# Optimization experiments

Hardware: AMD Instinct MI355X
Metric: run time of the kernel (lower is better)

## Reference

```python
import jax, jax.numpy as jnp
import numpy as np

VOCAB, EMB, HID = 50000, 128, 256
B, T = 64, 512


def setup_inputs() -> dict:
    key = jax.random.key(0)
    ks = jax.random.split(key, 10)
    node = jax.random.randint(ks[0], (B, T, 2), 0, VOCAB, dtype=jnp.int32)
    rel = jax.random.randint(ks[1], (B, T, 3), 0, VOCAB, dtype=jnp.int32)
    father = jax.random.randint(ks[2], (B, T), 0, T, dtype=jnp.int32)
    mask = jnp.ones((B, T), jnp.float32)
    # parameters (PyTorch LSTM layout: gates ordered i,f,g,o)
    embedding = jax.random.normal(ks[3], (VOCAB, EMB), jnp.float32) * 1e-4
    W_ih = jax.random.uniform(ks[4], (4 * HID, 2 * EMB), jnp.float32, -0.02, 0.02)
    W_hh = jax.random.uniform(ks[5], (4 * HID, HID), jnp.float32, -0.02, 0.02)
    b_ih = jnp.zeros((4 * HID,), jnp.float32).at[HID:2 * HID].set(1.0)  # forget bias = 1
    b_hh = jnp.zeros((4 * HID,), jnp.float32)
    W_h = jax.random.normal(ks[6], (HID, HID), jnp.float32) * 0.02
    return {"src_gtr_seq_node": node, "src_gtr_seq_rel": rel,
            "src_gtr_seq_father": father, "src_gtr_seq_node_mask": mask,
            "embedding": embedding, "W_ih": W_ih, "W_hh": W_hh,
            "b_ih": b_ih, "b_hh": b_hh, "W_h": W_h}


def reference(src_gtr_seq_node, src_gtr_seq_rel, src_gtr_seq_father,
              src_gtr_seq_node_mask, embedding, W_ih, W_hh, b_ih, b_hh, W_h):
    node, rel, father, mask = (src_gtr_seq_node, src_gtr_seq_rel,
                               src_gtr_seq_father, src_gtr_seq_node_mask)
    Bn, Tn = node.shape[:2]
    H = W_hh.shape[1]
    t_idx = jnp.arange(Tn, dtype=jnp.int32)
    # valid parent at step t must point into memory slots [0..t]; -1 -> zero root slot
    father = jnp.minimum(father, (t_idx - 1)[None, :])
    # 'avg' mode: mean of first-2 node token embeddings, mean of rel token embeddings
    node_e = embedding[node].mean(axis=2)            # [B,T,E]
    rel_e = embedding[rel].mean(axis=2)              # [B,T,E]
    x = jnp.concatenate([node_e, rel_e], axis=-1)    # [B,T,2E]
    gx = jnp.einsum('bte,ge->btg', x, W_ih) + b_ih   # [B,T,4H] input-side gates
    barange = jnp.arange(Bn)
    h_mem0 = jnp.zeros((Tn + 1, Bn, H), x.dtype)     # slot 0 = zero state (root)
    c_mem0 = jnp.zeros((Tn + 1, Bn, H), x.dtype)

    def step(carry, inp):
        h_mem, c_mem = carry
        t, gx_t, f_t = inp
        h_prev = h_mem[f_t + 1, barange]             # parent gather [B,H]
        c_prev = c_mem[f_t + 1, barange]
        gates = gx_t + h_prev @ W_hh.T + b_hh        # [B,4H]
        i, f, g, o = jnp.split(gates, 4, axis=-1)
        c = jax.nn.sigmoid(f) * c_prev + jax.nn.sigmoid(i) * jnp.tanh(g)
        h = jax.nn.sigmoid(o) * jnp.tanh(c)
        return (h_mem.at[t + 1].set(h), c_mem.at[t + 1].set(c)), h

    (h_mem, c_mem), outs = jax.lax.scan(
        step, (h_mem0, c_mem0),
        (t_idx, gx.transpose(1, 0, 2), father.T))
    m = mask[:, :, None]
    encoder_outputs = outs.transpose(1, 0, 2) * m    # [B,T,H]
    encoder_feature = encoder_outputs.reshape(-1, H) @ W_h.T  # [B*T,H]
    h_max = (h_mem[1:].transpose(1, 0, 2) * m).max(axis=1)[None]  # [1,B,H]
    c_max = (c_mem[1:].transpose(1, 0, 2) * m).max(axis=1)[None]
    return encoder_outputs, encoder_feature, h_max, c_max
```

## Files before the change

kernel.cpp:

```cpp
#include <hip/hip_runtime.h>
#include <hip/hip_bf16.h>
#include <math.h>

#define NB 64
#define NT 512
#define NH 256
#define NG 1024

typedef __bf16 bf16x8 __attribute__((ext_vector_type(8)));
typedef float  f32x4  __attribute__((ext_vector_type(4)));
typedef unsigned int u32x2 __attribute__((ext_vector_type(2)));

static __device__ __forceinline__ unsigned short f2bf(float x){
  __hip_bfloat16 h = __float2bfloat16(x);
  return __builtin_bit_cast(unsigned short, h);
}
static __device__ __forceinline__ float bf2f(unsigned short u){
  return __bfloat162float(__builtin_bit_cast(__hip_bfloat16, u));
}

#if __has_builtin(__builtin_amdgcn_sdot4)
#define SDOT4(a,b,c) __builtin_amdgcn_sdot4((a),(b),(c),false)
#else
static __device__ __forceinline__ int SDOT4(int a, int b, int c){
  c += ((a<<24)>>24)*((b<<24)>>24);
  c += ((a<<16)>>24)*((b<<16)>>24);
  c += ((a<< 8)>>24)*((b<< 8)>>24);
  c += ( a     >>24)*( b     >>24);
  return c;
}
#endif

#define QRED(x) do {                                                      \
    x += __builtin_amdgcn_update_dpp(0, x, 0xB1, 0xF, 0xF, true);         \
    x += __builtin_amdgcn_update_dpp(0, x, 0x4E, 0xF, 0xF, true);         \
  } while(0)

#define BAR_LGKM() asm volatile("s_waitcnt lgkmcnt(0)\n\ts_barrier" ::: "memory")
#define BAR_ALL()  asm volatile("s_waitcnt vmcnt(0) lgkmcnt(0)\n\ts_barrier" ::: "memory")

#define PIN(x) asm volatile("" : "+v"(x))

static __device__ __forceinline__ float tanh_acc(float x){
  float ax = fabsf(x);
  if (ax < 0.04f){
    float x2 = x*x;
    return x * (1.0f + x2*(-(1.0f/3.0f) + x2*(2.0f/15.0f)));
  }
  float e = __expf(-2.0f*ax);
  float r = (1.0f - e) / (1.0f + e);
  return copysignf(r, x);
}
static __device__ __forceinline__ float sigm(float x){
  return 1.0f / (1.0f + __expf(-x));
}

#define HSCALE 1270000.0f
#define WSCALE 6350.0f
#define DQ_CONST (1.0f/(HSCALE*WSCALE))

__global__ __launch_bounds__(256) void k_prep(
    const float* __restrict__ Wih, const float* __restrict__ Whh,
    const float* __restrict__ Wh,  const float* __restrict__ bih,
    const float* __restrict__ bhh,
    unsigned short* __restrict__ wih_bf, unsigned short* __restrict__ wh_bf,
    int* __restrict__ wq, float* __restrict__ bias)
{
  int i = blockIdx.x*256 + threadIdx.x;
  wih_bf[i] = f2bf(Wih[i]);
  if (i < 65536){
    wh_bf[i] = f2bf(Wh[i]);
    float4 wv = *(const float4*)(Whh + (long)i*4);
    int q0 = (int)rintf(wv.x * WSCALE); q0 = max(-127, min(127, q0));
    int q1 = (int)rintf(wv.y * WSCALE); q1 = max(-127, min(127, q1));
    int q2 = (int)rintf(wv.z * WSCALE); q2 = max(-127, min(127, q2));
    int q3 = (int)rintf(wv.w * WSCALE); q3 = max(-127, min(127, q3));
    int packed = (q0&255) | ((q1&255)<<8) | ((q2&255)<<16) | ((q3&255)<<24);
    int R = i >> 6, j = i & 63;
    int gate = R >> 8, ug = R & 255;
    int wv_ = ug >> 5, ul = ug & 31;
    int grp = ul >> 1, s = ul & 1;
    int ck = j >> 4, k = j & 15;
    int lane2 = grp*4 + ck;
    int r = gate*2 + s;
    wq[(((long)wv_*64 + lane2)*8 + r)*16 + k] = packed;
  }
  if (i < 1024) bias[i] = bih[i] + bhh[i];
}

__global__ __launch_bounds__(128) void k_x(
    const int* __restrict__ node, const int* __restrict__ rel,
    const float* __restrict__ emb, unsigned short* __restrict__ x)
{
  int bt = blockIdx.x; int e = threadIdx.x;
  int n0 = node[bt*2+0], n1 = node[bt*2+1];
  int r0 = rel[bt*3+0], r1 = rel[bt*3+1], r2 = rel[bt*3+2];
  float a = (emb[(long)n0*128+e] + emb[(long)n1*128+e]) * 0.5f;
  float b = (emb[(long)r0*128+e] + emb[(long)r1*128+e] + emb[(long)r2*128+e]) * (1.0f/3.0f);
  x[(long)bt*256 + e]       = f2bf(a);
  x[(long)bt*256 + 128 + e] = f2bf(b);
}

__global__ __launch_bounds__(256) void k_gemm(
    const unsigned short* __restrict__ A, const unsigned short* __restrict__ Bw,
    unsigned short* __restrict__ Cbf, float* __restrict__ Cf32,
    const float* __restrict__ mask, int N, int mode)
{
  __shared__ __align__(16) unsigned short As[64][32];
  __shared__ __align__(16) unsigned short Bs[64][32];
  const int tid = threadIdx.x;
  const int lane = tid & 63, wave = tid >> 6;
  const int wm = wave >> 1, wn = wave & 1;
  const int l15 = lane & 15, quad = lane >> 4;
  const int tM = blockIdx.x * 64, tN = blockIdx.y * 64;
  const int srow = tid >> 2, sseg = tid & 3;
  f32x4 acc[2][2] = {};
  long arow = tM + srow;
  if (mode == 1) arow = arow + (arow >> 9) + 1;
  const unsigned short* Aptr = A + arow*256 + sseg*8;
  const unsigned short* Bptr = Bw + (long)(tN + srow)*256 + sseg*8;
  for (int kc = 0; kc < 8; ++kc){
    bf16x8 av = *(const bf16x8*)(Aptr + kc*32);
    bf16x8 bv = *(const bf16x8*)(Bptr + kc*32);
    *(bf16x8*)&As[srow][sseg*8] = av;
    *(bf16x8*)&Bs[srow][sseg*8] = bv;
    __syncthreads();
    bf16x8 af[2], bg[2];
    #pragma unroll
    for (int i=0;i<2;++i) af[i] = *(const bf16x8*)&As[wm*32 + i*16 + l15][quad*8];
    #pragma unroll
    for (int j=0;j<2;++j) bg[j] = *(const bf16x8*)&Bs[wn*32 + j*16 + l15][quad*8];
    #pragma unroll
    for (int i=0;i<2;++i)
      #pragma unroll
      for (int j=0;j<2;++j)
        acc[i][j] = __builtin_amdgcn_mfma_f32_16x16x32_bf16(af[i], bg[j], acc[i][j], 0,0,0);
    __syncthreads();
  }
  #pragma unroll
  for (int i=0;i<2;++i)
  #pragma unroll
  for (int j=0;j<2;++j)
  #pragma unroll
  for (int r=0;r<4;++r){
    int m = tM + wm*32 + i*16 + quad*4 + r;
    int n = tN + wn*32 + j*16 + l15;
    float v = acc[i][j][r];
    if (mode == 0) Cbf[(long)m*1024 + ((n&255)<<2) + (n>>8)] = f2bf(v);
    else           Cf32[(long)m*N + n] = v * mask[m];
  }
}

__global__ __launch_bounds__(512, 1) void k_scan(
    const int* __restrict__ father, const unsigned short* __restrict__ gx,
    const int* __restrict__ wq_g, const float* __restrict__ bias,
    unsigned short* __restrict__ h_hist, float* __restrict__ c_hist)
{
  const int b    = blockIdx.x;
  const int tid  = threadIdx.x;
  const int lane = tid & 63;
  const int wave = tid >> 6;
  const int c4   = lane & 3;
  const int g16  = lane >> 2;
  const int s    = c4 & 1;
  const int u    = wave*32 + g16*2 + s;
  const int wrt  = (c4 < 2);
  extern __shared__ int smem[];
  int* hqh  = smem;
  int* fbuf = smem + 513*64;

  int w[128];
  {
    const int4* p = (const int4*)(wq_g + ((long)(wave*64 + lane))*128);
    #pragma unroll
    for (int j=0;j<32;++j){
      int4 v = p[j];
      w[4*j+0]=v.x; w[4*j+1]=v.y; w[4*j+2]=v.z; w[4*j+3]=v.w;
    }
  }
  #pragma unroll
  for (int j=0;j<128;++j) PIN(w[j]);

  const float bI = bias[u];
  const float bF = bias[256+u];
  const float bG = bias[512+u];
  const float bO = bias[768+u];
  fbuf[tid] = father[b*512 + tid];
  if (tid < 64) hqh[tid] = 0;

  const unsigned short* gxp = gx + (long)b*524288;
  u32x2 gv0 = *(const u32x2*)(gxp + (long)u*4);
  u32x2 gv1 = *(const u32x2*)(gxp + 1024 + (long)u*4);
  const unsigned short* gptr = gxp + 2*1024 + u*4;
  unsigned short* hst = h_hist + ((long)b*513 + 1)*256 + u;
  float*          cst = c_hist + ((long)b*513 + 1)*256 + u;
  const char*     clb = (const char*)(c_hist + (long)b*513*256 + u);

  float cpl0 = 0.f, cpl1 = 0.f;
  float cm1 = 0.f, cm2 = 0.f, cm3 = 0.f;
  float selv = 0.f; int useL = 0;
  int hbase = 0;
  int lastBar = -1;
  BAR_ALL();
  int fc1 = fbuf[1];

#define SCAN_BODY(T, CPL, GXV)                                                 \
  {                                                                            \
    const int t = (T);                                                         \
         \
    int4 ha = *(const int4*)&hqh[hbase + c4*16 + 0];                           \
    int4 hb = *(const int4*)&hqh[hbase + c4*16 + 4];                           \
    int4 hc = *(const int4*)&hqh[hbase + c4*16 + 8];                           \
    int4 hd = *(const int4*)&hqh[hbase + c4*16 + 12];                          \
    int acc[8] = {0,0,0,0,0,0,0,0};                                            \
    _Pragma("unroll")                                                          \
    for (int r=0;r<8;++r){                                                     \
      acc[r] = SDOT4(w[r*16+ 0], ha.x, acc[r]);                                \
      acc[r] = SDOT4(w[r*16+ 1], ha.y, acc[r]);                                \
      acc[r] = SDOT4(w[r*16+ 2], ha.z, acc[r]);                                \
      acc[r] = SDOT4(w[r*16+ 3], ha.w, acc[r]);                                \
      acc[r] = SDOT4(w[r*16+ 4], hb.x, acc[r]);                                \
      acc[r] = SDOT4(w[r*16+ 5], hb.y, acc[r]);                                \
      acc[r] = SDOT4(w[r*16+ 6], hb.z, acc[r]);                                \
      acc[r] = SDOT4(w[r*16+ 7], hb.w, acc[r]);                                \
      acc[r] = SDOT4(w[r*16+ 8], hc.x, acc[r]);                                \
      acc[r] = SDOT4(w[r*16+ 9], hc.y, acc[r]);                                \
      acc[r] = SDOT4(w[r*16+10], hc.z, acc[r]);                                \
      acc[r] = SDOT4(w[r*16+11], hc.w, acc[r]);                                \
      acc[r] = SDOT4(w[r*16+12], hd.x, acc[r]);                                \
      acc[r] = SDOT4(w[r*16+13], hd.y, acc[r]);                                \
      acc[r] = SDOT4(w[r*16+14], hd.z, acc[r]);                                \
      acc[r] = SDOT4(w[r*16+15], hd.w, acc[r]);                                \
    }                                                                          \
            \
    _Pragma("unroll")                                                          \
    for (int r=0;r<8;++r) QRED(acc[r]);                                        \
                  \
    asm volatile("s_waitcnt vmcnt(4)" : "+v"(CPL), "+v"(GXV));                 \
    float xi = __uint_as_float(GXV.x << 16);                                   \
    float xf = __uint_as_float(GXV.x & 0xFFFF0000u);                           \
    float xg = __uint_as_float(GXV.y << 16);                                   \
    float xo = __uint_as_float(GXV.y & 0xFFFF0000u);                           \
    int ai = s ? acc[1] : acc[0];                                              \
    int af = s ? acc[3] : acc[2];                                              \
    int ag = s ? acc[5] : acc[4];                                              \
    int ao = s ? acc[7] : acc[6];                                              \
    float vi = (float)ai * DQ_CONST + xi + bI;                                 \
    float vf = (float)af * DQ_CONST + xf + bF;                                 \
    float vg = (float)ag * DQ_CONST + xg + bG;                                 \
    float vo = (float)ao * DQ_CONST + xo + bO;                                 \
    float cp  = useL ? CPL : selv;                                             \
    float cc_ = fmaf(sigm(vf), cp, sigm(vi)*tanh_acc(vg));                     \
    float hh_ = sigm(vo)*tanh_acc(cc_);                                        \
    if (wrt){                                                                  \
      unsigned int hb16 = (unsigned int)f2bf(hh_);                             \
      asm volatile("global_store_short %0, %1, off" :: "v"(hst), "v"(hb16));   \
      asm volatile("global_store_dword %0, %1, off" :: "v"(cst), "v"(cc_));    \
      int q = (int)rintf(hh_ * HSCALE);                                        \
      q = max(-127, min(127, q));                                              \
      ((char*)hqh)[(t+1)*256 + u] = (char)q;                                   \
    }                                                                          \
    cm3 = cm2; cm2 = cm1; cm1 = cc_;                                           \
    hst += 256; cst += 256;                                                    \
              \
    int fr2 = __builtin_amdgcn_readfirstlane(fbuf[t+2 < 512 ? t+2 : 511]);     \
    {                                                                          \
      int fL = min(fr2, t+1);                                                  \
      const char* cla = clb + (long)(fL+1)*1024;                               \
      asm volatile("global_load_dword %0, %1, off" : "=v"(CPL) : "v"(cla));    \
      asm volatile("global_load_dwordx2 %0, %1, off" : "=v"(GXV) : "v"(gptr)); \
    }                                                                          \
    if (t < 509) gptr += 1024;                                                 \
            \
    {                                                                          \
      int fA = min(fc1, t);                                                    \
      useL = (fA < t-2);                                                       \
      selv = (fA == t) ? cm1 : ((fA == t-1) ? cm2 : cm3);                      \
      hbase = (fA + 1) * 64;                                                   \
      fc1 = fr2;                                                               \
      if (fA > lastBar){                                                       \
        BAR_LGKM();                                                            \
        lastBar = t;                                                           \
      }                                                                        \
    }                                                                          \
  }

  #pragma unroll 1
  for (int tb = 0; tb < 512; tb += 2){
    SCAN_BODY(tb,   cpl0, gv0)
    SCAN_BODY(tb+1, cpl1, gv1)
  }
#undef SCAN_BODY
}

__global__ __launch_bounds__(256) void k_eo1(
    const unsigned short* __restrict__ h_hist, const float* __restrict__ c_hist,
    const float* __restrict__ mask, float* __restrict__ out,
    float* __restrict__ pmax)
{
  int b = blockIdx.x, s = blockIdx.y, tid = threadIdx.x;
  float hm = -INFINITY, cm = -INFINITY;
  for (int i=0; i<64; ++i){
    int t = s*64 + i;
    long off = ((long)b*513 + t + 1)*256 + tid;
    float h = bf2f(h_hist[off]);
    float c = c_hist[off];
    float m = mask[b*512 + t];
    float e = h*m;
    out[((long)b*512 + t)*256 + tid] = e;
    hm = fmaxf(hm, e);
    cm = fmaxf(cm, c*m);
  }
  long po = ((long)(b*8 + s))*512 + tid;
  pmax[po]       = hm;
  pmax[po + 256] = cm;
}

__global__ __launch_bounds__(256) void k_eo2(
    const float* __restrict__ pmax, float* __restrict__ out)
{
  int b = blockIdx.x, tid = threadIdx.x;
  float hm = -INFINITY, cm = -INFINITY;
  for (int s=0; s<8; ++s){
    long po = ((long)(b*8 + s))*512 + tid;
    hm = fmaxf(hm, pmax[po]);
    cm = fmaxf(cm, pmax[po + 256]);
  }
  out[16777216L + b*256 + tid] = hm;
  out[16793600L + b*256 + tid] = cm;
}

extern "C" void kernel_launch(void* const* d_in, const int* in_sizes, int n_in,
                              void* d_out, int out_size, void* d_ws, size_t ws_size,
                              hipStream_t stream)
{
  const int*   node   = (const int*)  d_in[0];
  const int*   rel    = (const int*)  d_in[1];
  const int*   father = (const int*)  d_in[2];
  const float* mask   = (const float*)d_in[3];
  const float* emb    = (const float*)d_in[4];
  const float* Wih    = (const float*)d_in[5];
  const float* Whh    = (const float*)d_in[6];
  const float* bih    = (const float*)d_in[7];
  const float* bhh    = (const float*)d_in[8];
  const float* Wh     = (const float*)d_in[9];

  char* ws = (char*)d_ws;
  unsigned short* x_bf   = (unsigned short*)(ws);
  unsigned short* h_hist = (unsigned short*)(ws + 16777216);
  float*          c_hist = (float*)         (ws + 33587200);
  unsigned short* wih_bf = (unsigned short*)(ws + 75612160);
  unsigned short* wh_bf  = (unsigned short*)(ws + 76136448);
  int*            wq     = (int*)           (ws + 76267520);
  float*          bias   = (float*)         (ws + 76529664);
  float*          pmax   = (float*)(ws);

  unsigned short* gxbuf = (unsigned short*)d_out;
  float* out = (float*)d_out;

  const int scan_lds = (513*64 + 512)*4;

  k_prep<<<1024, 256, 0, stream>>>(Wih, Whh, Wh, bih, bhh, wih_bf, wh_bf, wq, bias);
  k_x<<<32768, 128, 0, stream>>>(node, rel, emb, x_bf);
  k_gemm<<<dim3(512,16), 256, 0, stream>>>(x_bf, wih_bf, gxbuf, nullptr, nullptr, 1024, 0);
  k_scan<<<64, 512, scan_lds, stream>>>(father, gxbuf, wq, bias, h_hist, c_hist);
  k_gemm<<<dim3(512,4), 256, 0, stream>>>(h_hist, wh_bf, nullptr, out + 8388608, mask, 256, 1);
  k_eo1<<<dim3(64,8), 256, 0, stream>>>(h_hist, c_hist, mask, out, pmax);
  k_eo2<<<64, 256, 0, stream>>>(pmax, out);
}
```

Measured before the change: 779.1 us.

## Use int8 MFMA for recurrent W_hh matvec in LSTM scan kernel

Replaces the per-lane sdot4 dot products plus DPP reductions in the sequential scan with int8 16x16x64 MFMA instructions. The quantized W_hh is repacked in the prep kernel into MFMA A-fragment layout held in registers, and the parent hidden vector is read as the B operand. Each lane then picks its unit's gate value out of the accumulator with selects. This removes the cross-lane reduction and cuts instruction count on the serial critical path. The cost is that the MFMA computes 16 columns where only one is useful, and the MFMA latency sits on each step's dependency chain.

```diff
diff --git a/kernel.cpp b/kernel.cpp
--- a/kernel.cpp
+++ b/kernel.cpp
@@ -9,6 +9,7 @@
 
 typedef __bf16 bf16x8 __attribute__((ext_vector_type(8)));
 typedef float  f32x4  __attribute__((ext_vector_type(4)));
+typedef int    i32x4  __attribute__((ext_vector_type(4)));
 typedef unsigned int u32x2 __attribute__((ext_vector_type(2)));
 
 static __device__ __forceinline__ unsigned short f2bf(float x){
@@ -18,23 +19,6 @@
 static __device__ __forceinline__ float bf2f(unsigned short u){
   return __bfloat162float(__builtin_bit_cast(__hip_bfloat16, u));
 }
-
-#if __has_builtin(__builtin_amdgcn_sdot4)
-#define SDOT4(a,b,c) __builtin_amdgcn_sdot4((a),(b),(c),false)
-#else
-static __device__ __forceinline__ int SDOT4(int a, int b, int c){
-  c += ((a<<24)>>24)*((b<<24)>>24);
-  c += ((a<<16)>>24)*((b<<16)>>24);
-  c += ((a<< 8)>>24)*((b<< 8)>>24);
-  c += ( a     >>24)*( b     >>24);
-  return c;
-}
-#endif
-
-#define QRED(x) do {                                                      \
-    x += __builtin_amdgcn_update_dpp(0, x, 0xB1, 0xF, 0xF, true);         \
-    x += __builtin_amdgcn_update_dpp(0, x, 0x4E, 0xF, 0xF, true);         \
-  } while(0)
 
 #define BAR_LGKM() asm volatile("s_waitcnt lgkmcnt(0)\n\ts_barrier" ::: "memory")
 #define BAR_ALL()  asm volatile("s_waitcnt vmcnt(0) lgkmcnt(0)\n\ts_barrier" ::: "memory")
@@ -70,20 +54,24 @@
   wih_bf[i] = f2bf(Wih[i]);
   if (i < 65536){
     wh_bf[i] = f2bf(Wh[i]);
-    float4 wv = *(const float4*)(Whh + (long)i*4);
+    int o  = i;
+    int dw   = o & 3;
+    int o1   = o >> 2;
+    int lane = o1 & 63;
+    int o2   = o1 >> 6;
+    int kc   = o2 & 3;
+    int o3   = o2 >> 2;
+    int tile = o3 & 7;
+    int w    = (o3 >> 3) & 7;
+    int g = tile >> 1, p = tile & 1;
+    int row = g*256 + w*32 + p*16 + (lane & 15);
+    int kb  = kc*64 + (lane >> 4)*16 + dw*4;
+    float4 wv = *(const float4*)(Whh + (long)row*256 + kb);
     int q0 = (int)rintf(wv.x * WSCALE); q0 = max(-127, min(127, q0));
     int q1 = (int)rintf(wv.y * WSCALE); q1 = max(-127, min(127, q1));
     int q2 = (int)rintf(wv.z * WSCALE); q2 = max(-127, min(127, q2));
     int q3 = (int)rintf(wv.w * WSCALE); q3 = max(-127, min(127, q3));
-    int packed = (q0&255) | ((q1&255)<<8) | ((q2&255)<<16) | ((q3&255)<<24);
-    int R = i >> 6, j = i & 63;
-    int gate = R >> 8, ug = R & 255;
-    int wv_ = ug >> 5, ul = ug & 31;
-    int grp = ul >> 1, s = ul & 1;
-    int ck = j >> 4, k = j & 15;
-    int lane2 = grp*4 + ck;
-    int r = gate*2 + s;
-    wq[(((long)wv_*64 + lane2)*8 + r)*16 + k] = packed;
+    wq[o] = (q0&255) | ((q1&255)<<8) | ((q2&255)<<16) | ((q3&255)<<24);
   }
   if (i < 1024) bias[i] = bih[i] + bhh[i];
 }
@@ -160,26 +148,36 @@
   const int tid  = threadIdx.x;
   const int lane = tid & 63;
   const int wave = tid >> 6;
-  const int c4   = lane & 3;
-  const int g16  = lane >> 2;
-  const int s    = c4 & 1;
-  const int u    = wave*32 + g16*2 + s;
-  const int wrt  = (c4 < 2);
+  const int c15  = lane & 15;
+  const int quad = lane >> 4;
+  const int koff = quad * 16;
+  const int ps   = (c15 >> 3) & 1;
+  const int rsel = (c15 >> 1) & 3;
+  const int u    = wave*32 + ps*16 + quad*4 + rsel;
+  const int wrt  = ((c15 & 1) == 0);
   extern __shared__ int smem[];
   int* hqh  = smem;
   int* fbuf = smem + 513*64;
 
-  int w[128];
+  i32x4 afr[4][2][4];
   {
-    const int4* p = (const int4*)(wq_g + ((long)(wave*64 + lane))*128);
-    #pragma unroll
-    for (int j=0;j<32;++j){
-      int4 v = p[j];
-      w[4*j+0]=v.x; w[4*j+1]=v.y; w[4*j+2]=v.z; w[4*j+3]=v.w;
-    }
+    const i32x4* wp = (const i32x4*)wq_g;
+    #pragma unroll
+    for (int g=0; g<4; ++g)
+      #pragma unroll
+      for (int p=0; p<2; ++p)
+        #pragma unroll
+        for (int kc=0; kc<4; ++kc)
+          afr[g][p][kc] = wp[((wave*8 + g*2+p)*4 + kc)*64 + lane];
   }
   #pragma unroll
-  for (int j=0;j<128;++j) PIN(w[j]);
+  for (int g=0; g<4; ++g)
+    #pragma unroll
+    for (int p=0; p<2; ++p)
+      #pragma unroll
+      for (int kc=0; kc<4; ++kc){
+        PIN(afr[g][p][kc]);
+      }
 
   const float bI = bias[u];
   const float bF = bias[256+u];
@@ -199,56 +197,57 @@
   float cpl0 = 0.f, cpl1 = 0.f;
   float cm1 = 0.f, cm2 = 0.f, cm3 = 0.f;
   float selv = 0.f; int useL = 0;
-  int hbase = 0;
+  int hbyte = 0;
   int lastBar = -1;
   BAR_ALL();
   int fc1 = fbuf[1];
+
+#define GSEL(g, out) {                                                         \
+    int e0 = (rsel & 1) ? acc[g][0][1] : acc[g][0][0];                         \
+    int e1 = (rsel & 1) ? acc[g][0][3] : acc[g][0][2];                         \
+    int e2 = (rsel & 1) ? acc[g][1][1] : acc[g][1][0];                         \
+    int e3 = (rsel & 1) ? acc[g][1][3] : acc[g][1][2];                         \
+    int f0 = (rsel & 2) ? e1 : e0;                                             \
+    int f1 = (rsel & 2) ? e3 : e2;                                             \
+    out = ps ? f1 : f0; }
 
 #define SCAN_BODY(T, CPL, GXV)                                                 \
   {                                                                            \
     const int t = (T);                                                         \
          \
-    int4 ha = *(const int4*)&hqh[hbase + c4*16 + 0];                           \
-    int4 hb = *(const int4*)&hqh[hbase + c4*16 + 4];                           \
-    int4 hc = *(const int4*)&hqh[hbase + c4*16 + 8];                           \
-    int4 hd = *(const int4*)&hqh[hbase + c4*16 + 12];                          \
-    int acc[8] = {0,0,0,0,0,0,0,0};                                            \
+    const char* hrow = (const char*)hqh + hbyte;                               \
+    i32x4 bq0 = *(const i32x4*)(hrow +   0 + koff);                            \
+    i32x4 bq1 = *(const i32x4*)(hrow +  64 + koff);                            \
+    i32x4 bq2 = *(const i32x4*)(hrow + 128 + koff);                            \
+    i32x4 bq3 = *(const i32x4*)(hrow + 192 + koff);                            \
+    i32x4 acc[4][2];                                                           \
+    const i32x4 zz = {0,0,0,0};                                                \
     _Pragma("unroll")                                                          \
-    for (int r=0;r<8;++r){                                                     \
-      acc[r] = SDOT4(w[r*16+ 0], ha.x, acc[r]);                                \
-      acc[r] = SDOT4(w[r*16+ 1], ha.y, acc[r]);                                \
-      acc[r] = SDOT4(w[r*16+ 2], ha.z, acc[r]);                                \
-      acc[r] = SDOT4(w[r*16+ 3], ha.w, acc[r]);                                \
-      acc[r] = SDOT4(w[r*16+ 4], hb.x, acc[r]);                                \
-      acc[r] = SDOT4(w[r*16+ 5], hb.y, acc[r]);                                \
-      acc[r] = SDOT4(w[r*16+ 6], hb.z, acc[r]);                                \
-      acc[r] = SDOT4(w[r*16+ 7], hb.w, acc[r]);                                \
-      acc[r] = SDOT4(w[r*16+ 8], hc.x, acc[r]);                                \
-      acc[r] = SDOT4(w[r*16+ 9], hc.y, acc[r]);                                \
-      acc[r] = SDOT4(w[r*16+10], hc.z, acc[r]);                                \
-      acc[r] = SDOT4(w[r*16+11], hc.w, acc[r]);                                \
-      acc[r] = SDOT4(w[r*16+12], hd.x, acc[r]);                                \
-      acc[r] = SDOT4(w[r*16+13], hd.y, acc[r]);                                \
-      acc[r] = SDOT4(w[r*16+14], hd.z, acc[r]);                                \
-      acc[r] = SDOT4(w[r*16+15], hd.w, acc[r]);                                \
-    }                                                                          \
-            \
+    for (int g=0; g<4; ++g)                                                    \
+      _Pragma("unroll")                                                        \
+      for (int p=0; p<2; ++p)                                                  \
+        acc[g][p] = __builtin_amdgcn_mfma_i32_16x16x64_i8(afr[g][p][0], bq0, zz, 0,0,0); \
     _Pragma("unroll")                                                          \
-    for (int r=0;r<8;++r) QRED(acc[r]);                                        \
+    for (int g=0; g<4; ++g)                                                    \
+      _Pragma("unroll")                                                        \
+      for (int p=0; p<2; ++p){                                                 \
+        acc[g][p] = __builtin_amdgcn_mfma_i32_16x16x64_i8(afr[g][p][1], bq1, acc[g][p], 0,0,0); \
+        acc[g][p] = __builtin_amdgcn_mfma_i32_16x16x64_i8(afr[g][p][2], bq2, acc[g][p], 0,0,0); \
+        acc[g][p] = __builtin_amdgcn_mfma_i32_16x16x64_i8(afr[g][p][3], bq3, acc[g][p], 0,0,0); \
+      }                                                                        \
+                  \
+    int ai, af_, ag, ao;                                                       \
+    GSEL(0, ai) GSEL(1, af_) GSEL(2, ag) GSEL(3, ao)                           \
                   \
     asm volatile("s_waitcnt vmcnt(4)" : "+v"(CPL), "+v"(GXV));                 \
     float xi = __uint_as_float(GXV.x << 16);                                   \
     float xf = __uint_as_float(GXV.x & 0xFFFF0000u);                           \
     float xg = __uint_as_float(GXV.y << 16);                                   \
     float xo = __uint_as_float(GXV.y & 0xFFFF0000u);                           \
-    int ai = s ? acc[1] : acc[0];                                              \
-    int af = s ? acc[3] : acc[2];                                              \
-    int ag = s ? acc[5] : acc[4];                                              \
-    int ao = s ? acc[7] : acc[6];                                              \
-    float vi = (float)ai * DQ_CONST + xi + bI;                                 \
-    float vf = (float)af * DQ_CONST + xf + bF;                                 \
-    float vg = (float)ag * DQ_CONST + xg + bG;                                 \
-    float vo = (float)ao * DQ_CONST + xo + bO;                                 \
+    float vi = (float)ai  * DQ_CONST + xi + bI;                                \
+    float vf = (float)af_ * DQ_CONST + xf + bF;                                \
+    float vg = (float)ag  * DQ_CONST + xg + bG;                                \
+    float vo = (float)ao  * DQ_CONST + xo + bO;                                \
     float cp  = useL ? CPL : selv;                                             \
     float cc_ = fmaf(sigm(vf), cp, sigm(vi)*tanh_acc(vg));                     \
     float hh_ = sigm(vo)*tanh_acc(cc_);                                        \
@@ -276,7 +275,7 @@
       int fA = min(fc1, t);                                                    \
       useL = (fA < t-2);                                                       \
       selv = (fA == t) ? cm1 : ((fA == t-1) ? cm2 : cm3);                      \
-      hbase = (fA + 1) * 64;                                                   \
+      hbyte = (fA + 1) * 256;                                                  \
       fc1 = fr2;                                                               \
       if (fA > lastBar){                                                       \
         BAR_LGKM();                                                            \
@@ -291,6 +290,7 @@
     SCAN_BODY(tb+1, cpl1, gv1)
   }
 #undef SCAN_BODY
+#undef GSEL
 }
 
 __global__ __launch_bounds__(256) void k_eo1(
```

After: 716.0 us. 8.1% less time.
